# Kernel tuning notes

Measured on AMD Instinct MI355X. Metric: run time of the kernel, lower is better.

Reference implementation:

```python
import jax, jax.numpy as jnp
import numpy as np

EPS = 1e-6
COEF_CLIP = 120.0
ACTIVE_IDX = 0


def setup_inputs() -> dict:
    key = jax.random.key(0)
    ks = jax.random.split(key, 7)
    A, T, H = 4, 8192, 2048
    return {
        "hidden_states": jax.random.normal(ks[0], (A, T, H), dtype=jnp.float32),
        "activated": jax.random.normal(ks[1], (T, H), dtype=jnp.float32),
        "router_norm_weight": jax.random.uniform(ks[2], (H,), dtype=jnp.float32),
        "w_router": jax.random.normal(ks[3], (A, H), dtype=jnp.float32),
        "w_pred": jax.random.normal(ks[4], (A * A, A), dtype=jnp.float32),
        "w_corr": jax.random.normal(ks[5], (A, A), dtype=jnp.float32),
        "correct_output_scale": jax.random.normal(ks[6], (H,), dtype=jnp.float32),
    }


def reference(hidden_states, activated, router_norm_weight, w_router, w_pred,
              w_corr, correct_output_scale):
    A, T, H = hidden_states.shape
    router_input_scale = 1.0 / H

    def rmsnorm(x):
        xf = x.astype(jnp.float32)
        var = jnp.mean(xf * xf, axis=-1, keepdims=True)
        return (xf * jax.lax.rsqrt(var + EPS)) * router_norm_weight

    def modalities(x):
        # [T, H] -> [T, A]
        r = rmsnorm(x) * router_input_scale
        return jnp.tanh(r @ w_router.T)

    # ---- predict ----
    m_pred = modalities(hidden_states[ACTIVE_IDX])                 # [T, A]
    wp = jnp.clip(w_pred, -COEF_CLIP, COEF_CLIP)                   # [A*A, A]
    # reshape [T, A, A] then permute(0, 2, 1)
    all_coefs = (m_pred @ wp.T).reshape(T, A, A).transpose(0, 2, 1)
    # matmul(hs.permute(1,2,0)[T,H,A], all_coefs[T,A,B]) -> permute(2,0,1) -> [B,T,H]
    predictions = jnp.einsum('ath,tab->bth', hidden_states, all_coefs)
    predictions = predictions + hidden_states                      # [A, T, H]

    # ---- correct ----
    m_corr = modalities(activated)                                 # [T, A]
    wc = jnp.clip(w_corr, -COEF_CLIP, COEF_CLIP)                   # [A, A]
    cc = (m_corr @ wc.T) + 1.0                                     # [T, A]
    innovation = activated - predictions[ACTIVE_IDX]               # [T, H]
    corrected = innovation[None, :, :] * cc.T[:, :, None] + predictions  # [A,T,H]

    # ---- scale active output ----
    output = corrected[ACTIVE_IDX] * correct_output_scale          # [T, H]
    return corrected, output
```

## Files before the change

### kernel.cpp

```cpp
#include <hip/hip_runtime.h>
#include <math.h>

namespace {

typedef float f32x4 __attribute__((ext_vector_type(4)));

constexpr int A = 4;
constexpr int H = 2048;
constexpr int BLK = 256;
constexpr float EPSV = 1e-6f;
constexpr float CLIPV = 120.0f;

__device__ __forceinline__ float clipv(float v) {
    return fminf(fmaxf(v, -CLIPV), CLIPV);
}

__global__ __launch_bounds__(BLK) void altup_fused(
    const float* __restrict__ hs,
    const float* __restrict__ act,
    const float* __restrict__ rnw,
    const float* __restrict__ w_router,
    const float* __restrict__ w_pred,
    const float* __restrict__ w_corr,
    const float* __restrict__ oscale,
    float* __restrict__ out,
    int T)
{
    const int t   = blockIdx.x;
    const int tid = threadIdx.x;
    const size_t TH = (size_t)T * H;
    const size_t rowOff = (size_t)t * H;
    const int hofs[2] = {tid * 4, 1024 + tid * 4};

    f32x4 x0[2], av[2], x1[2], x2[2], x3[2], rv[2], sv[2], wr[4][2];
#pragma unroll
    for (int c = 0; c < 2; ++c) {
        const int h = hofs[c];
        x0[c] = __builtin_nontemporal_load((const f32x4*)(hs + rowOff + h));
        av[c] = __builtin_nontemporal_load((const f32x4*)(act + rowOff + h));
        x1[c] = __builtin_nontemporal_load((const f32x4*)(hs + 1 * TH + rowOff + h));
        x2[c] = __builtin_nontemporal_load((const f32x4*)(hs + 2 * TH + rowOff + h));
        x3[c] = __builtin_nontemporal_load((const f32x4*)(hs + 3 * TH + rowOff + h));
        rv[c] = *(const f32x4*)(rnw + h);
        sv[c] = *(const f32x4*)(oscale + h);
#pragma unroll
        for (int j = 0; j < 4; ++j)
            wr[j][c] = *(const f32x4*)(w_router + j * H + h);
    }

    float part[10];
#pragma unroll
    for (int i = 0; i < 10; ++i) part[i] = 0.f;

#pragma unroll
    for (int c = 0; c < 2; ++c) {
#pragma unroll
        for (int k = 0; k < 4; ++k) {
            const float x = x0[c][k], a = av[c][k], r = rv[c][k];
            part[0] = fmaf(x, x, part[0]);
            part[5] = fmaf(a, a, part[5]);
            const float xr = x * r;
            const float ar = a * r;
            part[1] = fmaf(xr, wr[0][c][k], part[1]);
            part[2] = fmaf(xr, wr[1][c][k], part[2]);
            part[3] = fmaf(xr, wr[2][c][k], part[3]);
            part[4] = fmaf(xr, wr[3][c][k], part[4]);
            part[6] = fmaf(ar, wr[0][c][k], part[6]);
            part[7] = fmaf(ar, wr[1][c][k], part[7]);
            part[8] = fmaf(ar, wr[2][c][k], part[8]);
            part[9] = fmaf(ar, wr[3][c][k], part[9]);
        }
    }

#pragma unroll
    for (int off = 32; off >= 1; off >>= 1) {
#pragma unroll
        for (int i = 0; i < 10; ++i) part[i] += __shfl_down(part[i], off, 64);
    }

    __shared__ float red[BLK / 64][10];
    const int wave = tid >> 6;
    const int lane = tid & 63;
    if (lane == 0) {
#pragma unroll
        for (int i = 0; i < 10; ++i) red[wave][i] = part[i];
    }
    __syncthreads();

    float sums[10];
#pragma unroll
    for (int i = 0; i < 10; ++i)
        sums[i] = red[0][i] + red[1][i] + red[2][i] + red[3][i];

    const float invH = 1.0f / (float)H;
    const float sp = rsqrtf(sums[0] * invH + EPSV) * invH;
    const float sc = rsqrtf(sums[5] * invH + EPSV) * invH;
    float mp[4], mc[4];
#pragma unroll
    for (int j = 0; j < 4; ++j) {
        mp[j] = tanhf(sums[1 + j] * sp);
        mc[j] = tanhf(sums[6 + j] * sc);
    }

    float coef[4][4];
#pragma unroll
    for (int b = 0; b < 4; ++b) {
#pragma unroll
        for (int a = 0; a < 4; ++a) {
            float s = 0.f;
#pragma unroll
            for (int j = 0; j < 4; ++j)
                s = fmaf(mp[j], clipv(w_pred[(b * 4 + a) * A + j]), s);
            coef[a][b] = s;
        }
    }
    float cc[4];
#pragma unroll
    for (int a = 0; a < 4; ++a) {
        float s = 1.0f;
#pragma unroll
        for (int j = 0; j < 4; ++j)
            s = fmaf(mc[j], clipv(w_corr[a * A + j]), s);
        cc[a] = s;
    }

#pragma unroll
    for (int c = 0; c < 2; ++c) {
        const int h = hofs[c];
        f32x4 co[4], ov;
#pragma unroll
        for (int k = 0; k < 4; ++k) {
            const float xs4[4] = {x0[c][k], x1[c][k], x2[c][k], x3[c][k]};
            float pr[4];
#pragma unroll
            for (int b = 0; b < 4; ++b) {
                float s = xs4[b];
#pragma unroll
                for (int a = 0; a < 4; ++a)
                    s = fmaf(xs4[a], coef[a][b], s);
                pr[b] = s;
            }
            const float innov = av[c][k] - pr[0];
#pragma unroll
            for (int a = 0; a < 4; ++a)
                co[a][k] = fmaf(innov, cc[a], pr[a]);
            ov[k] = co[0][k] * sv[c][k];
        }
#pragma unroll
        for (int a = 0; a < 4; ++a)
            __builtin_nontemporal_store(co[a], (f32x4*)(out + (size_t)a * TH + rowOff + h));
        __builtin_nontemporal_store(ov, (f32x4*)(out + (size_t)A * TH + rowOff + h));
    }
}

}

extern "C" void kernel_launch(void* const* d_in, const int* in_sizes, int n_in,
                              void* d_out, int out_size, void* d_ws, size_t ws_size,
                              hipStream_t stream) {
    const float* hs       = (const float*)d_in[0];
    const float* act      = (const float*)d_in[1];
    const float* rnw      = (const float*)d_in[2];
    const float* w_router = (const float*)d_in[3];
    const float* w_pred   = (const float*)d_in[4];
    const float* w_corr   = (const float*)d_in[5];
    const float* oscale   = (const float*)d_in[6];
    float* out = (float*)d_out;

    const int T = in_sizes[1] / H;

    altup_fused<<<dim3(T), dim3(BLK), 0, stream>>>(
        hs, act, rnw, w_router, w_pred, w_corr, oscale, out, T);
}
```

Measured before the change: 124.6 us.

## Process four tokens per block with double-buffered register prefetch

Each block now handles four tokens strided by the grid size instead of one. The loads for the next token are issued into a second register buffer before the current token is reduced and written, and shared reduction slots are double-buffered so each token needs one barrier. The aim is to amortise the per-block setup loads of the weight and scale vectors and to overlap memory latency with the reduction. The launch bound now asks for two blocks per SIMD, and the doubled register buffers raise register pressure. T must be divisible by 4.

```diff
diff --git a/kernel.cpp b/kernel.cpp
--- a/kernel.cpp
+++ b/kernel.cpp
@@ -8,6 +8,7 @@
 constexpr int A = 4;
 constexpr int H = 2048;
 constexpr int BLK = 256;
+constexpr int TPB = 4;
 constexpr float EPSV = 1e-6f;
 constexpr float CLIPV = 120.0f;
 
@@ -15,7 +16,7 @@
     return fminf(fmaxf(v, -CLIPV), CLIPV);
 }
 
-__global__ __launch_bounds__(BLK) void altup_fused(
+__global__ __launch_bounds__(BLK, 2) void altup_fused(
     const float* __restrict__ hs,
     const float* __restrict__ act,
     const float* __restrict__ rnw,
@@ -24,23 +25,17 @@
     const float* __restrict__ w_corr,
     const float* __restrict__ oscale,
     float* __restrict__ out,
-    int T)
+    int T, int G)
 {
-    const int t   = blockIdx.x;
+    const int b   = blockIdx.x;
     const int tid = threadIdx.x;
     const size_t TH = (size_t)T * H;
-    const size_t rowOff = (size_t)t * H;
     const int hofs[2] = {tid * 4, 1024 + tid * 4};
 
-    f32x4 x0[2], av[2], x1[2], x2[2], x3[2], rv[2], sv[2], wr[4][2];
+    f32x4 rv[2], sv[2], wr[4][2];
 #pragma unroll
     for (int c = 0; c < 2; ++c) {
         const int h = hofs[c];
-        x0[c] = __builtin_nontemporal_load((const f32x4*)(hs + rowOff + h));
-        av[c] = __builtin_nontemporal_load((const f32x4*)(act + rowOff + h));
-        x1[c] = __builtin_nontemporal_load((const f32x4*)(hs + 1 * TH + rowOff + h));
-        x2[c] = __builtin_nontemporal_load((const f32x4*)(hs + 2 * TH + rowOff + h));
-        x3[c] = __builtin_nontemporal_load((const f32x4*)(hs + 3 * TH + rowOff + h));
         rv[c] = *(const f32x4*)(rnw + h);
         sv[c] = *(const f32x4*)(oscale + h);
 #pragma unroll
@@ -48,109 +43,136 @@
             wr[j][c] = *(const f32x4*)(w_router + j * H + h);
     }
 
-    float part[10];
-#pragma unroll
-    for (int i = 0; i < 10; ++i) part[i] = 0.f;
+    f32x4 s[2][2][5];
+
+#define LDTOK(i, p)                                                              \
+    {                                                                            \
+        const size_t ro = (size_t)(b + (i) * G) * H;                             \
+        _Pragma("unroll")                                                        \
+        for (int c = 0; c < 2; ++c) {                                            \
+            const int h = hofs[c];                                               \
+            s[p][c][0] = __builtin_nontemporal_load((const f32x4*)(hs + ro + h));            \
+            s[p][c][1] = __builtin_nontemporal_load((const f32x4*)(act + ro + h));           \
+            s[p][c][2] = __builtin_nontemporal_load((const f32x4*)(hs + 1 * TH + ro + h));   \
+            s[p][c][3] = __builtin_nontemporal_load((const f32x4*)(hs + 2 * TH + ro + h));   \
+            s[p][c][4] = __builtin_nontemporal_load((const f32x4*)(hs + 3 * TH + ro + h));   \
+        }                                                                        \
+    }
+
+    __shared__ float red[2][10][BLK / 64];
+    const int wave = tid >> 6;
+    const int lane = tid & 63;
+    const float invH = 1.0f / (float)H;
+
+    LDTOK(0, 0);
 
 #pragma unroll
-    for (int c = 0; c < 2; ++c) {
+    for (int i = 0; i < TPB; ++i) {
+        const int p = i & 1;
+        if (i + 1 < TPB) LDTOK(i + 1, p ^ 1);
+
+        float part[10];
 #pragma unroll
-        for (int k = 0; k < 4; ++k) {
-            const float x = x0[c][k], a = av[c][k], r = rv[c][k];
-            part[0] = fmaf(x, x, part[0]);
-            part[5] = fmaf(a, a, part[5]);
-            const float xr = x * r;
-            const float ar = a * r;
-            part[1] = fmaf(xr, wr[0][c][k], part[1]);
-            part[2] = fmaf(xr, wr[1][c][k], part[2]);
-            part[3] = fmaf(xr, wr[2][c][k], part[3]);
-            part[4] = fmaf(xr, wr[3][c][k], part[4]);
-            part[6] = fmaf(ar, wr[0][c][k], part[6]);
-            part[7] = fmaf(ar, wr[1][c][k], part[7]);
-            part[8] = fmaf(ar, wr[2][c][k], part[8]);
-            part[9] = fmaf(ar, wr[3][c][k], part[9]);
+        for (int q = 0; q < 10; ++q) part[q] = 0.f;
+#pragma unroll
+        for (int c = 0; c < 2; ++c) {
+#pragma unroll
+            for (int k = 0; k < 4; ++k) {
+                const float x = s[p][c][0][k], a = s[p][c][1][k], r = rv[c][k];
+                part[0] = fmaf(x, x, part[0]);
+                part[5] = fmaf(a, a, part[5]);
+                const float xr = x * r;
+                const float ar = a * r;
+                part[1] = fmaf(xr, wr[0][c][k], part[1]);
+                part[2] = fmaf(xr, wr[1][c][k], part[2]);
+                part[3] = fmaf(xr, wr[2][c][k], part[3]);
+                part[4] = fmaf(xr, wr[3][c][k], part[4]);
+                part[6] = fmaf(ar, wr[0][c][k], part[6]);
+                part[7] = fmaf(ar, wr[1][c][k], part[7]);
+                part[8] = fmaf(ar, wr[2][c][k], part[8]);
+                part[9] = fmaf(ar, wr[3][c][k], part[9]);
+            }
+        }
+
+#pragma unroll
+        for (int off = 32; off >= 1; off >>= 1) {
+#pragma unroll
+            for (int q = 0; q < 10; ++q) part[q] += __shfl_down(part[q], off, 64);
+        }
+        if (lane == 0) {
+#pragma unroll
+            for (int q = 0; q < 10; ++q) red[p][q][wave] = part[q];
+        }
+        __syncthreads();
+
+        float sums[10];
+#pragma unroll
+        for (int q = 0; q < 10; ++q) {
+            const f32x4 v = *(const f32x4*)&red[p][q][0];
+            sums[q] = (v[0] + v[1]) + (v[2] + v[3]);
+        }
+
+        const float spn = rsqrtf(sums[0] * invH + EPSV) * invH;
+        const float scn = rsqrtf(sums[5] * invH + EPSV) * invH;
+        float mp[4], mc[4];
+#pragma unroll
+        for (int j = 0; j < 4; ++j) {
+            mp[j] = tanhf(sums[1 + j] * spn);
+            mc[j] = tanhf(sums[6 + j] * scn);
+        }
+        float coef[4][4];
+#pragma unroll
+        for (int bb = 0; bb < 4; ++bb) {
+#pragma unroll
+            for (int aa = 0; aa < 4; ++aa) {
+                float sacc = 0.f;
+#pragma unroll
+                for (int j = 0; j < 4; ++j)
+                    sacc = fmaf(mp[j], clipv(w_pred[(bb * 4 + aa) * A + j]), sacc);
+                coef[aa][bb] = sacc;
+            }
+        }
+        float cc[4];
+#pragma unroll
+        for (int aa = 0; aa < 4; ++aa) {
+            float sacc = 1.0f;
+#pragma unroll
+            for (int j = 0; j < 4; ++j)
+                sacc = fmaf(mc[j], clipv(w_corr[aa * A + j]), sacc);
+            cc[aa] = sacc;
+        }
+
+        const size_t ro = (size_t)(b + i * G) * H;
+#pragma unroll
+        for (int c = 0; c < 2; ++c) {
+            const int h = hofs[c];
+            f32x4 co[4], ov;
+#pragma unroll
+            for (int k = 0; k < 4; ++k) {
+                const float xs4[4] = {s[p][c][0][k], s[p][c][2][k],
+                                      s[p][c][3][k], s[p][c][4][k]};
+                float pr[4];
+#pragma unroll
+                for (int bb = 0; bb < 4; ++bb) {
+                    float sacc = xs4[bb];
+#pragma unroll
+                    for (int aa = 0; aa < 4; ++aa)
+                        sacc = fmaf(xs4[aa], coef[aa][bb], sacc);
+                    pr[bb] = sacc;
+                }
+                const float innov = s[p][c][1][k] - pr[0];
+#pragma unroll
+                for (int aa = 0; aa < 4; ++aa)
+                    co[aa][k] = fmaf(innov, cc[aa], pr[aa]);
+                ov[k] = co[0][k] * sv[c][k];
+            }
+#pragma unroll
+            for (int aa = 0; aa < 4; ++aa)
+                __builtin_nontemporal_store(co[aa], (f32x4*)(out + (size_t)aa * TH + ro + h));
+            __builtin_nontemporal_store(ov, (f32x4*)(out + (size_t)A * TH + ro + h));
         }
     }
-
-#pragma unroll
-    for (int off = 32; off >= 1; off >>= 1) {
-#pragma unroll
-        for (int i = 0; i < 10; ++i) part[i] += __shfl_down(part[i], off, 64);
-    }
-
-    __shared__ float red[BLK / 64][10];
-    const int wave = tid >> 6;
-    const int lane = tid & 63;
-    if (lane == 0) {
-#pragma unroll
-        for (int i = 0; i < 10; ++i) red[wave][i] = part[i];
-    }
-    __syncthreads();
-
-    float sums[10];
-#pragma unroll
-    for (int i = 0; i < 10; ++i)
-        sums[i] = red[0][i] + red[1][i] + red[2][i] + red[3][i];
-
-    const float invH = 1.0f / (float)H;
-    const float sp = rsqrtf(sums[0] * invH + EPSV) * invH;
-    const float sc = rsqrtf(sums[5] * invH + EPSV) * invH;
-    float mp[4], mc[4];
-#pragma unroll
-    for (int j = 0; j < 4; ++j) {
-        mp[j] = tanhf(sums[1 + j] * sp);
-        mc[j] = tanhf(sums[6 + j] * sc);
-    }
-
-    float coef[4][4];
-#pragma unroll
-    for (int b = 0; b < 4; ++b) {
-#pragma unroll
-        for (int a = 0; a < 4; ++a) {
-            float s = 0.f;
-#pragma unroll
-            for (int j = 0; j < 4; ++j)
-                s = fmaf(mp[j], clipv(w_pred[(b * 4 + a) * A + j]), s);
-            coef[a][b] = s;
-        }
-    }
-    float cc[4];
-#pragma unroll
-    for (int a = 0; a < 4; ++a) {
-        float s = 1.0f;
-#pragma unroll
-        for (int j = 0; j < 4; ++j)
-            s = fmaf(mc[j], clipv(w_corr[a * A + j]), s);
-        cc[a] = s;
-    }
-
-#pragma unroll
-    for (int c = 0; c < 2; ++c) {
-        const int h = hofs[c];
-        f32x4 co[4], ov;
-#pragma unroll
-        for (int k = 0; k < 4; ++k) {
-            const float xs4[4] = {x0[c][k], x1[c][k], x2[c][k], x3[c][k]};
-            float pr[4];
-#pragma unroll
-            for (int b = 0; b < 4; ++b) {
-                float s = xs4[b];
-#pragma unroll
-                for (int a = 0; a < 4; ++a)
-                    s = fmaf(xs4[a], coef[a][b], s);
-                pr[b] = s;
-            }
-            const float innov = av[c][k] - pr[0];
-#pragma unroll
-            for (int a = 0; a < 4; ++a)
-                co[a][k] = fmaf(innov, cc[a], pr[a]);
-            ov[k] = co[0][k] * sv[c][k];
-        }
-#pragma unroll
-        for (int a = 0; a < 4; ++a)
-            __builtin_nontemporal_store(co[a], (f32x4*)(out + (size_t)a * TH + rowOff + h));
-        __builtin_nontemporal_store(ov, (f32x4*)(out + (size_t)A * TH + rowOff + h));
-    }
+#undef LDTOK
 }
 
 }
@@ -168,7 +190,8 @@
     float* out = (float*)d_out;
 
     const int T = in_sizes[1] / H;
+    const int G = T / TPB;
 
-    altup_fused<<<dim3(T), dim3(BLK), 0, stream>>>(
-        hs, act, rnw, w_router, w_pred, w_corr, oscale, out, T);
+    altup_fused<<<dim3(G), dim3(BLK), 0, stream>>>(
+        hs, act, rnw, w_router, w_pred, w_corr, oscale, out, T, G);
 }
```

Measured after the change: 127.3 us. 1.02x slower.

## Split fused kernel into per-row coefficient kernel and streaming apply kernel

Applied to the files above, without the earlier changes.

Splits the single fused kernel into two. A one-wave-per-row kernel computes the RMS-norm router reductions, prediction coefficients and correction coefficients, and writes them to workspace. A second kernel streams the elementwise predict/correct pass using those precomputed coefficients. The reduction is processed in reverse row order so that the hs[0] and activated rows it reads last are still in cache when the apply kernel re-reads them from the start. The goal is to remove the block-wide barrier and reduction from the bandwidth-bound apply pass. The cost is reading hs[0] and activated twice plus an extra kernel launch. The original fused kernel is kept as a fallback when the workspace is too small.

```diff
diff --git a/kernel.cpp b/kernel.cpp
--- a/kernel.cpp
+++ b/kernel.cpp
@@ -7,7 +7,6 @@
 
 constexpr int A = 4;
 constexpr int H = 2048;
-constexpr int BLK = 256;
 constexpr float EPSV = 1e-6f;
 constexpr float CLIPV = 120.0f;
 
@@ -15,16 +14,159 @@
     return fminf(fmaxf(v, -CLIPV), CLIPV);
 }
 
-__global__ __launch_bounds__(BLK) void altup_fused(
+__device__ __forceinline__ f32x4 vfma(float s, f32x4 w, f32x4 acc) {
+    f32x4 r;
+#pragma unroll
+    for (int i = 0; i < 4; ++i) r[i] = fmaf(s, w[i], acc[i]);
+    return r;
+}
+
+__global__ __launch_bounds__(64, 4) void coef_kernel(
     const float* __restrict__ hs,
     const float* __restrict__ act,
     const float* __restrict__ rnw,
     const float* __restrict__ w_router,
     const float* __restrict__ w_pred,
     const float* __restrict__ w_corr,
+    float* __restrict__ coefs,
+    int T)
+{
+    const int t = T - 1 - (int)blockIdx.x;
+    const int lane = threadIdx.x;
+    const size_t ro = (size_t)t * H;
+
+    float part[10];
+#pragma unroll
+    for (int q = 0; q < 10; ++q) part[q] = 0.f;
+
+#pragma unroll
+    for (int c = 0; c < 8; ++c) {
+        const int h = c * 256 + lane * 4;
+        const f32x4 x  = *(const f32x4*)(hs + ro + h);
+        const f32x4 a  = *(const f32x4*)(act + ro + h);
+        const f32x4 r  = *(const f32x4*)(rnw + h);
+        const f32x4 w0 = *(const f32x4*)(w_router + 0 * H + h);
+        const f32x4 w1 = *(const f32x4*)(w_router + 1 * H + h);
+        const f32x4 w2 = *(const f32x4*)(w_router + 2 * H + h);
+        const f32x4 w3 = *(const f32x4*)(w_router + 3 * H + h);
+#pragma unroll
+        for (int k = 0; k < 4; ++k) {
+            const float xv = x[k], av = a[k], rv = r[k];
+            part[0] = fmaf(xv, xv, part[0]);
+            part[5] = fmaf(av, av, part[5]);
+            const float xr = xv * rv;
+            const float ar = av * rv;
+            part[1] = fmaf(xr, w0[k], part[1]);
+            part[2] = fmaf(xr, w1[k], part[2]);
+            part[3] = fmaf(xr, w2[k], part[3]);
+            part[4] = fmaf(xr, w3[k], part[4]);
+            part[6] = fmaf(ar, w0[k], part[6]);
+            part[7] = fmaf(ar, w1[k], part[7]);
+            part[8] = fmaf(ar, w2[k], part[8]);
+            part[9] = fmaf(ar, w3[k], part[9]);
+        }
+    }
+
+#pragma unroll
+    for (int off = 32; off >= 1; off >>= 1) {
+#pragma unroll
+        for (int q = 0; q < 10; ++q) part[q] += __shfl_xor(part[q], off, 64);
+    }
+
+    const float invH = 1.0f / (float)H;
+    const float sp = rsqrtf(part[0] * invH + EPSV) * invH;
+    const float sc = rsqrtf(part[5] * invH + EPSV) * invH;
+    float mp[4], mc[4];
+#pragma unroll
+    for (int j = 0; j < 4; ++j) {
+        mp[j] = tanhf(part[1 + j] * sp);
+        mc[j] = tanhf(part[6 + j] * sc);
+    }
+
+    float coef[4][4], cc[4];
+#pragma unroll
+    for (int bb = 0; bb < 4; ++bb)
+#pragma unroll
+        for (int aa = 0; aa < 4; ++aa) {
+            float s = 0.f;
+#pragma unroll
+            for (int j = 0; j < 4; ++j)
+                s = fmaf(mp[j], clipv(w_pred[(bb * 4 + aa) * A + j]), s);
+            coef[aa][bb] = s;
+        }
+#pragma unroll
+    for (int aa = 0; aa < 4; ++aa) {
+        float s = 1.0f;
+#pragma unroll
+        for (int j = 0; j < 4; ++j)
+            s = fmaf(mc[j], clipv(w_corr[aa * A + j]), s);
+        cc[aa] = s;
+    }
+
+    float* dst = coefs + (size_t)t * 20;
+    if (lane < 16)      dst[lane] = coef[lane >> 2][lane & 3];
+    else if (lane < 20) dst[lane] = cc[lane - 16];
+}
+
+__global__ __launch_bounds__(256, 4) void apply_kernel(
+    const float* __restrict__ hs,
+    const float* __restrict__ act,
     const float* __restrict__ oscale,
+    const float* __restrict__ coefs,
     float* __restrict__ out,
     int T)
+{
+    const int t   = blockIdx.x;
+    const int tid = threadIdx.x;
+    const size_t TH = (size_t)T * H;
+    const size_t ro = (size_t)t * H;
+
+    const float* cf = coefs + (size_t)t * 20;
+    const f32x4 cf0 = *(const f32x4*)(cf + 0);
+    const f32x4 cf1 = *(const f32x4*)(cf + 4);
+    const f32x4 cf2 = *(const f32x4*)(cf + 8);
+    const f32x4 cf3 = *(const f32x4*)(cf + 12);
+    const f32x4 ccv = *(const f32x4*)(cf + 16);
+
+#pragma unroll
+    for (int c = 0; c < 2; ++c) {
+        const int h = c * 1024 + tid * 4;
+        const f32x4 x0 = *(const f32x4*)(hs + ro + h);
+        const f32x4 av = *(const f32x4*)(act + ro + h);
+        const f32x4 x1 = __builtin_nontemporal_load((const f32x4*)(hs + 1 * TH + ro + h));
+        const f32x4 x2 = __builtin_nontemporal_load((const f32x4*)(hs + 2 * TH + ro + h));
+        const f32x4 x3 = __builtin_nontemporal_load((const f32x4*)(hs + 3 * TH + ro + h));
+        const f32x4 sv = *(const f32x4*)(oscale + h);
+
+        f32x4 co0, co1, co2, co3, ov;
+#pragma unroll
+        for (int k = 0; k < 4; ++k) {
+            const f32x4 xs = {x0[k], x1[k], x2[k], x3[k]};
+            f32x4 pr = xs;
+            pr = vfma(xs[0], cf0, pr);
+            pr = vfma(xs[1], cf1, pr);
+            pr = vfma(xs[2], cf2, pr);
+            pr = vfma(xs[3], cf3, pr);
+            const float innov = av[k] - pr[0];
+            co0[k] = fmaf(innov, ccv[0], pr[0]);
+            co1[k] = fmaf(innov, ccv[1], pr[1]);
+            co2[k] = fmaf(innov, ccv[2], pr[2]);
+            co3[k] = fmaf(innov, ccv[3], pr[3]);
+            ov[k] = co0[k] * sv[k];
+        }
+        __builtin_nontemporal_store(co0, (f32x4*)(out + 0 * TH + ro + h));
+        __builtin_nontemporal_store(co1, (f32x4*)(out + 1 * TH + ro + h));
+        __builtin_nontemporal_store(co2, (f32x4*)(out + 2 * TH + ro + h));
+        __builtin_nontemporal_store(co3, (f32x4*)(out + 3 * TH + ro + h));
+        __builtin_nontemporal_store(ov,  (f32x4*)(out + (size_t)A * TH + ro + h));
+    }
+}
+
+__global__ __launch_bounds__(256) void altup_fused(
+    const float* __restrict__ hs, const float* __restrict__ act,
+    const float* __restrict__ rnw, const float* __restrict__ w_router,
+    const float* __restrict__ w_pred, const float* __restrict__ w_corr,
+    const float* __restrict__ oscale, float* __restrict__ out, int T)
 {
     const int t   = blockIdx.x;
     const int tid = threadIdx.x;
@@ -44,23 +186,19 @@
         rv[c] = *(const f32x4*)(rnw + h);
         sv[c] = *(const f32x4*)(oscale + h);
 #pragma unroll
-        for (int j = 0; j < 4; ++j)
-            wr[j][c] = *(const f32x4*)(w_router + j * H + h);
-    }
-
+        for (int j = 0; j < 4; ++j) wr[j][c] = *(const f32x4*)(w_router + j * H + h);
+    }
     float part[10];
 #pragma unroll
     for (int i = 0; i < 10; ++i) part[i] = 0.f;
-
-#pragma unroll
-    for (int c = 0; c < 2; ++c) {
+#pragma unroll
+    for (int c = 0; c < 2; ++c)
 #pragma unroll
         for (int k = 0; k < 4; ++k) {
             const float x = x0[c][k], a = av[c][k], r = rv[c][k];
             part[0] = fmaf(x, x, part[0]);
             part[5] = fmaf(a, a, part[5]);
-            const float xr = x * r;
-            const float ar = a * r;
+            const float xr = x * r, ar = a * r;
             part[1] = fmaf(xr, wr[0][c][k], part[1]);
             part[2] = fmaf(xr, wr[1][c][k], part[2]);
             part[3] = fmaf(xr, wr[2][c][k], part[3]);
@@ -70,28 +208,20 @@
             part[8] = fmaf(ar, wr[2][c][k], part[8]);
             part[9] = fmaf(ar, wr[3][c][k], part[9]);
         }
-    }
-
-#pragma unroll
-    for (int off = 32; off >= 1; off >>= 1) {
+#pragma unroll
+    for (int off = 32; off >= 1; off >>= 1)
 #pragma unroll
         for (int i = 0; i < 10; ++i) part[i] += __shfl_down(part[i], off, 64);
-    }
-
-    __shared__ float red[BLK / 64][10];
-    const int wave = tid >> 6;
-    const int lane = tid & 63;
-    if (lane == 0) {
+    __shared__ float red[4][10];
+    const int wave = tid >> 6, lane = tid & 63;
+    if (lane == 0)
 #pragma unroll
         for (int i = 0; i < 10; ++i) red[wave][i] = part[i];
-    }
     __syncthreads();
-
     float sums[10];
 #pragma unroll
     for (int i = 0; i < 10; ++i)
         sums[i] = red[0][i] + red[1][i] + red[2][i] + red[3][i];
-
     const float invH = 1.0f / (float)H;
     const float sp = rsqrtf(sums[0] * invH + EPSV) * invH;
     const float sc = rsqrtf(sums[5] * invH + EPSV) * invH;
@@ -101,29 +231,23 @@
         mp[j] = tanhf(sums[1 + j] * sp);
         mc[j] = tanhf(sums[6 + j] * sc);
     }
-
-    float coef[4][4];
-#pragma unroll
-    for (int b = 0; b < 4; ++b) {
+    float coef[4][4], cc[4];
+#pragma unroll
+    for (int b = 0; b < 4; ++b)
 #pragma unroll
         for (int a = 0; a < 4; ++a) {
             float s = 0.f;
 #pragma unroll
-            for (int j = 0; j < 4; ++j)
-                s = fmaf(mp[j], clipv(w_pred[(b * 4 + a) * A + j]), s);
+            for (int j = 0; j < 4; ++j) s = fmaf(mp[j], clipv(w_pred[(b * 4 + a) * A + j]), s);
             coef[a][b] = s;
         }
-    }
-    float cc[4];
 #pragma unroll
     for (int a = 0; a < 4; ++a) {
         float s = 1.0f;
 #pragma unroll
-        for (int j = 0; j < 4; ++j)
-            s = fmaf(mc[j], clipv(w_corr[a * A + j]), s);
+        for (int j = 0; j < 4; ++j) s = fmaf(mc[j], clipv(w_corr[a * A + j]), s);
         cc[a] = s;
     }
-
 #pragma unroll
     for (int c = 0; c < 2; ++c) {
         const int h = hofs[c];
@@ -136,14 +260,12 @@
             for (int b = 0; b < 4; ++b) {
                 float s = xs4[b];
 #pragma unroll
-                for (int a = 0; a < 4; ++a)
-                    s = fmaf(xs4[a], coef[a][b], s);
+                for (int a = 0; a < 4; ++a) s = fmaf(xs4[a], coef[a][b], s);
                 pr[b] = s;
             }
             const float innov = av[c][k] - pr[0];
 #pragma unroll
-            for (int a = 0; a < 4; ++a)
-                co[a][k] = fmaf(innov, cc[a], pr[a]);
+            for (int a = 0; a < 4; ++a) co[a][k] = fmaf(innov, cc[a], pr[a]);
             ov[k] = co[0][k] * sv[c][k];
         }
 #pragma unroll
@@ -168,7 +290,16 @@
     float* out = (float*)d_out;
 
     const int T = in_sizes[1] / H;
-
-    altup_fused<<<dim3(T), dim3(BLK), 0, stream>>>(
-        hs, act, rnw, w_router, w_pred, w_corr, oscale, out, T);
-}
+    const size_t need = (size_t)T * 20 * sizeof(float);
+
+    if (ws_size >= need) {
+        float* coefs = (float*)d_ws;
+        coef_kernel<<<dim3(T), dim3(64), 0, stream>>>(
+            hs, act, rnw, w_router, w_pred, w_corr, coefs, T);
+        apply_kernel<<<dim3(T), dim3(256), 0, stream>>>(
+            hs, act, oscale, coefs, out, T);
+    } else {
+        altup_fused<<<dim3(T), dim3(256), 0, stream>>>(
+            hs, act, rnw, w_router, w_pred, w_corr, oscale, out, T);
+    }
+}
```

Measured after the change: 141.6 us. 1.14x slower.
